# Optimization experiments

Measured on AMD Instinct MI355X. Metric: run time of the kernel, lower is better.

Reference implementation:

```python
import jax, jax.numpy as jnp
import numpy as np

N = 50000        # nodes
E = 800000       # random edges (plus N self-loops added in setup)
DIN = 128        # input_dim
H = 128          # hidden_dim
L = 3            # num_layers
EPS = 1e-5       # BatchNorm1d eps


def _bn(x, gamma, beta):
    # BatchNorm1d in training mode: batch stats over node axis, biased variance
    m = x.mean(axis=0)
    v = jnp.mean((x - m) ** 2, axis=0)
    return (x - m) * jax.lax.rsqrt(v + EPS) * gamma + beta


def setup_inputs() -> dict:
    key = jax.random.key(0)
    ks = jax.random.split(key, 11)
    feats = jax.random.normal(ks[0], (N, DIN), dtype=jnp.float32)
    # edge list with self-loops so every node has degree >= 1 (average pooling divides by degree)
    loops = jnp.arange(N, dtype=jnp.int64)
    src = jnp.concatenate([jax.random.randint(ks[1], (E,), 0, N, dtype=jnp.int64), loops])
    dst = jnp.concatenate([jax.random.randint(ks[2], (E,), 0, N, dtype=jnp.int64), loops])
    s = 0.05
    # per-layer MLP params (num_mlp_layers=2: Linear -> BN -> ReLU -> Linear), layer 0 has DIN==H
    W1 = jax.random.normal(ks[3], (L, DIN, H), dtype=jnp.float32) * s
    b1 = jnp.zeros((L, H), jnp.float32)
    g1 = jnp.ones((L, H), jnp.float32)
    be1 = jnp.zeros((L, H), jnp.float32)
    W2 = jax.random.normal(ks[4], (L, H, H), dtype=jnp.float32) * s
    b2 = jnp.zeros((L, H), jnp.float32)
    # outer BatchNorm1d per GNN layer
    og = jnp.ones((L, H), jnp.float32)
    ob = jnp.zeros((L, H), jnp.float32)
    return {"feats": feats, "W1": W1, "b1": b1, "g1": g1, "be1": be1,
            "W2": W2, "b2": b2, "og": og, "ob": ob, "src": src, "dst": dst}


def reference(feats, W1, b1, g1, be1, W2, b2, og, ob, src, dst):
    n = feats.shape[0]
    # degree = spmm(Adj, ones) -- constant across layers
    deg = jax.ops.segment_sum(jnp.ones(src.shape, jnp.float32), dst, num_segments=n)[:, None]
    h = feats
    for l in range(L):
        # pooled = spmm(Adj, h) via edge gather + segment reduce, then 'average' normalize
        pooled = jax.ops.segment_sum(h[src], dst, num_segments=n) / deg
        # GIN-style 2-layer MLP: Linear -> BN -> ReLU -> Linear
        z = jax.nn.relu(_bn(pooled @ W1[l] + b1[l], g1[l], be1[l]))
        z = z @ W2[l] + b2[l]
        # outer BatchNorm + ReLU
        h = jax.nn.relu(_bn(z, og[l], ob[l]))
    return h
```

## Files before the change

kernel.cpp:

```cpp
#include <hip/hip_runtime.h>
#include <hip/hip_bf16.h>
#include <stdint.h>

typedef _Float16 h16;
typedef h16 h16x2 __attribute__((ext_vector_type(2)));
typedef h16 h16x8 __attribute__((ext_vector_type(8)));
typedef float f32x4 __attribute__((ext_vector_type(4)));

#define HF 128
#define EPS 1e-5f
#define BSH 9
#define BROWS 512
#define BCAP 16384
#define ECHUNK 8192
#define SBANKS 8

union pk32 { uint32_t u; h16x2 h; };

static __device__ __forceinline__ uint32_t pack_h16(float a, float b) {
    pk32 c;
    c.h[0] = (h16)a; c.h[1] = (h16)b;
    return c.u;
}

static __device__ __forceinline__ float sum8(const float* __restrict__ st, int idx) {
    float s = 0.f;
#pragma unroll
    for (int b = 0; b < SBANKS; b++) s += st[b * 256 + idx];
    return s;
}


__global__ __launch_bounds__(256) void k_bscatter(const int* __restrict__ src,
                                                  const int* __restrict__ dst,
                                                  int* __restrict__ gcursor,
                                                  int2* __restrict__ staging, int ne, int nb) {
    __shared__ int h[128], gb[128];
    const int tid = threadIdx.x;
    if (tid < nb) h[tid] = 0;
    __syncthreads();
    const int beg = blockIdx.x * ECHUNK;
    const int end = min(beg + ECHUNK, ne);
    for (int i = beg + tid; i < end; i += 256)
        atomicAdd(&h[dst[i] >> BSH], 1);
    __syncthreads();
    if (tid < nb) {
        int c = h[tid];
        gb[tid] = c ? atomicAdd(&gcursor[tid], c) : 0;
        h[tid] = 0;
    }
    __syncthreads();
    for (int i = beg + tid; i < end; i += 256) {
        int d = dst[i];
        int b = d >> BSH;
        int r = atomicAdd(&h[b], 1);
        staging[(size_t)b * BCAP + gb[b] + r] = make_int2(src[i], d);
    }
}

__global__ __launch_bounds__(256) void k_bbuild(const int2* __restrict__ staging,
                                                const int* __restrict__ gcursor,
                                                int* __restrict__ rowbeg,
                                                int* __restrict__ rowend,
                                                float* __restrict__ deginv,
                                                int* __restrict__ csrsrc, int n) {
    __shared__ int hist[BROWS];
    __shared__ int scan[BROWS];
    const int b = blockIdx.x;
    const int tid = threadIdx.x;
    const int rb = b << BSH;
    const int nrows = min(BROWS, n - rb);
    const int base = b * BCAP;
    const int cnt = gcursor[b];
    hist[tid] = 0; hist[tid + 256] = 0;
    __syncthreads();
    for (int i = tid; i < cnt; i += 256)
        atomicAdd(&hist[staging[base + i].y - rb], 1);
    __syncthreads();
    const int i0 = tid, i1 = tid + 256;
    scan[i0] = hist[i0]; scan[i1] = hist[i1];
    __syncthreads();
    for (int off = 1; off < BROWS; off <<= 1) {
        int v0 = (i0 >= off) ? scan[i0 - off] : 0;
        int v1 = (i1 >= off) ? scan[i1 - off] : 0;
        __syncthreads();
        scan[i0] += v0; scan[i1] += v1;
        __syncthreads();
    }
    for (int r = tid; r < BROWS; r += 256) {
        int c = hist[r];
        int excl = scan[r] - c;
        if (r < nrows) {
            rowbeg[rb + r] = base + excl;
            rowend[rb + r] = base + excl + c;
            deginv[rb + r] = c ? 1.0f / (float)c : 0.f;
        }
        scan[r] = excl;
    }
    __syncthreads();
    for (int i = tid; i < cnt; i += 256) {
        int2 e = staging[base + i];
        int pos = atomicAdd(&scan[e.y - rb], 1);
        csrsrc[base + pos] = e.x;
    }
}

__global__ __launch_bounds__(256) void k_prep(const float* __restrict__ W1,
                                              const float* __restrict__ W2,
                                              h16* __restrict__ wp,
                                              const float* __restrict__ feats,
                                              uint32_t* __restrict__ hbuf, long tot2) {
    const int bid = (int)blockIdx.x;
    if (bid < 384) {
        const int mat = bid >> 6;
        const int idx = ((bid & 63) << 8) + (int)threadIdx.x;
        const int l = mat >> 1;
        const float* Wsrc = (mat & 1) ? (W2 + l * 16384) : (W1 + l * 16384);
        const int nn = idx >> 7, k = idx & 127;
        float w = Wsrc[k * 128 + nn];
        int pos = nn * 128 + ((((k >> 3) ^ (nn & 7))) << 3) + (k & 7);
        wp[mat * 16384 + pos] = (h16)w;
    } else {
        long i = (long)(bid - 384) * 256 + threadIdx.x;
        if (i < tot2) {
            float2 v = ((const float2*)feats)[i];
            hbuf[i] = pack_h16(v.x, v.y);
        }
    }
}

template <int AFF>
__global__ __launch_bounds__(256) void k_spmm(const uint32_t* __restrict__ hp,
                                              const int* __restrict__ rowbeg,
                                              const int* __restrict__ rowend,
                                              const float* __restrict__ deginv,
                                              const float* __restrict__ st,
                                              const float* __restrict__ g,
                                              const float* __restrict__ be,
                                              float inv_n,
                                              const int* __restrict__ csrsrc,
                                              uint32_t* __restrict__ pooled, int n, int np) {
    const int wid  = (int)((blockIdx.x * 256u + threadIdx.x) >> 6);
    const int lane = threadIdx.x & 63;
    if (wid >= np) return;
    uint32_t* outp = pooled + (size_t)wid * 64 + lane;
    if (wid >= n) { *outp = 0u; return; }
    h16x2 s2 = (h16x2)(h16)1.f, c2 = (h16x2)(h16)0.f;
    if (AFF) {
        const int c0 = lane * 2, c1 = c0 + 1;
        float m0 = sum8(st, c0) * inv_n, v0 = sum8(st, 128 + c0) * inv_n - m0 * m0;
        float sx = g[c0] * rsqrtf(v0 + EPS), cx = be[c0] - m0 * sx;
        float m1 = sum8(st, c1) * inv_n, v1 = sum8(st, 128 + c1) * inv_n - m1 * m1;
        float sy = g[c1] * rsqrtf(v1 + EPS), cy = be[c1] - m1 * sy;
        s2[0] = (h16)sx; s2[1] = (h16)sy;
        c2[0] = (h16)cx; c2[1] = (h16)cy;
    }
    const h16 z0 = (h16)0.f;
    h16x2 acc = (h16x2)z0;
    const int beg = rowbeg[wid], end = rowend[wid];
    for (int base = beg; base < end; base += 64) {
        const int rem = end - base;
        const int cnt = rem < 64 ? rem : 64;
        const int off = lane < cnt ? lane : cnt - 1;
        const int idx = csrsrc[base + off];
        int j = 0;
        for (; j + 8 <= cnt; j += 8) {
            uint32_t p[8];
#pragma unroll
            for (int u = 0; u < 8; u++) {
                int s = __builtin_amdgcn_readlane(idx, j + u);
                p[u] = hp[(size_t)s * 64 + lane];
            }
#pragma unroll
            for (int u = 0; u < 8; u++) {
                pk32 w; w.u = p[u];
                h16x2 v = w.h;
                if (AFF) {
                    v = v * s2 + c2;
                    v[0] = v[0] > z0 ? v[0] : z0;
                    v[1] = v[1] > z0 ? v[1] : z0;
                }
                acc = acc + v;
            }
        }
        for (; j < cnt; j++) {
            int s = __builtin_amdgcn_readlane(idx, j);
            pk32 w; w.u = hp[(size_t)s * 64 + lane];
            h16x2 v = w.h;
            if (AFF) {
                v = v * s2 + c2;
                v[0] = v[0] > z0 ? v[0] : z0;
                v[1] = v[1] > z0 ? v[1] : z0;
            }
            acc = acc + v;
        }
    }
    const float di = deginv[wid];
    *outp = pack_h16((float)acc[0] * di, (float)acc[1] * di);
}

template <int MODE>
__global__ __launch_bounds__(256) void k_gemm(const uint32_t* __restrict__ Ap,
                                              const h16* __restrict__ Wp,
                                              const float* __restrict__ bias,
                                              const float* __restrict__ st,
                                              const float* __restrict__ g,
                                              const float* __restrict__ be,
                                              float inv_n,
                                              h16* __restrict__ Y,
                                              float* __restrict__ outstats, int n) {
    __shared__ __align__(16) h16 WT[128 * 128];
    __shared__ float sred[4][128];
    __shared__ float sred2[4][128];
    __shared__ float aff[256];
    const int tid = threadIdx.x;
    const int wave = tid >> 6, lane = tid & 63;

    {
        const char* gsrc = (const char*)Wp + wave * 1024 + lane * 16;
        char* ldst = (char*)&WT[0] + wave * 1024;
#pragma unroll
        for (int i = 0; i < 8; i++) {
            __builtin_amdgcn_global_load_lds(
                (const __attribute__((address_space(1))) uint32_t*)(gsrc + i * 4096),
                (__attribute__((address_space(3))) uint32_t*)(ldst + i * 4096),
                16, 0, 0);
        }
    }
    if (MODE == 1 && tid < 128) {
        float m = sum8(st, tid) * inv_n;
        float v = sum8(st, 128 + tid) * inv_n - m * m;
        float a = g[tid] * rsqrtf(v + EPS);
        aff[tid] = a;
        aff[128 + tid] = be[tid] - m * a;
    }

    const int lrow = lane & 15, quad = lane >> 4;
    const int bx = (int)blockIdx.x * 128;
    int mb[2];
    mb[0] = bx + wave * 16;
    mb[1] = bx + 64 + wave * 16;

    h16x8 ah[2][4];
    uint4 araw[2][4];
#pragma unroll
    for (int rt = 0; rt < 2; rt++) {
        const uint32_t* arow = Ap + (size_t)(mb[rt] + lrow) * 64 + quad * 4;
#pragma unroll
        for (int kt = 0; kt < 4; kt++)
            araw[rt][kt] = *(const uint4*)(arow + kt * 16);
    }

    __syncthreads();

#pragma unroll
    for (int rt = 0; rt < 2; rt++) {
#pragma unroll
        for (int kt = 0; kt < 4; kt++) {
            if (MODE == 0) {
                ah[rt][kt] = *(const h16x8*)&araw[rt][kt];
            } else {
                const uint32_t* pw = (const uint32_t*)&araw[rt][kt];
                h16x8 t;
#pragma unroll
                for (int j2 = 0; j2 < 4; j2++) {
                    pk32 w; w.u = pw[j2];
                    int k = kt * 32 + quad * 8 + j2 * 2;
                    float x0 = fmaxf(fmaf((float)w.h[0], aff[k],     aff[128 + k]),     0.f);
                    float x1 = fmaxf(fmaf((float)w.h[1], aff[k + 1], aff[129 + k]), 0.f);
                    t[2 * j2]     = (h16)x0;
                    t[2 * j2 + 1] = (h16)x1;
                }
                ah[rt][kt] = t;
            }
        }
    }

    f32x4 acc[2][8];
#pragma unroll
    for (int rt = 0; rt < 2; rt++)
#pragma unroll
        for (int nt = 0; nt < 8; nt++) acc[rt][nt] = (f32x4){0.f, 0.f, 0.f, 0.f};

    const int sw = lrow & 7;
#pragma unroll
    for (int nt = 0; nt < 8; nt++) {
        const h16* wbase = &WT[(nt * 16 + lrow) * 128];
#pragma unroll
        for (int kt = 0; kt < 4; kt++) {
            h16x8 bh = *(const h16x8*)(wbase + (((4 * kt + quad) ^ sw) << 3));
#pragma unroll
            for (int rt = 0; rt < 2; rt++)
                acc[rt][nt] = __builtin_amdgcn_mfma_f32_16x16x32_f16(ah[rt][kt], bh, acc[rt][nt], 0, 0, 0);
        }
    }

#pragma unroll
    for (int nt = 0; nt < 8; nt++) {
        int col = nt * 16 + lrow;
        float bv = bias[col];
        float csum = 0.f, csq = 0.f;
#pragma unroll
        for (int rt = 0; rt < 2; rt++) {
#pragma unroll
            for (int r = 0; r < 4; r++) {
                int row = mb[rt] + quad * 4 + r;
                float yv = acc[rt][nt][r] + bv;
                Y[(size_t)row * 128 + col] = (h16)yv;
                if (row < n) { csum += yv; csq += yv * yv; }
            }
        }
        csum += __shfl_xor(csum, 16, 64); csum += __shfl_xor(csum, 32, 64);
        csq  += __shfl_xor(csq,  16, 64); csq  += __shfl_xor(csq,  32, 64);
        if (quad == 0) { sred[wave][col] = csum; sred2[wave][col] = csq; }
    }
    __syncthreads();
    if (tid < 128) {
        float s = sred[0][tid] + sred[1][tid] + sred[2][tid] + sred[3][tid];
        float q = sred2[0][tid] + sred2[1][tid] + sred2[2][tid] + sred2[3][tid];
        const int bank = (int)(blockIdx.x & (SBANKS - 1));
        atomicAdd(&outstats[bank * 256 + tid], s);
        atomicAdd(&outstats[bank * 256 + 128 + tid], q);
    }
}

__global__ __launch_bounds__(256) void k_bnrelu(const uint32_t* __restrict__ Z,
                                                const float* __restrict__ st,
                                                const float* __restrict__ g,
                                                const float* __restrict__ be,
                                                float inv_n,
                                                float* __restrict__ out, long tot2) {
    long i = (long)blockIdx.x * 256 + threadIdx.x;
    if (i >= tot2) return;
    int c = (int)((i * 2) & 127);
    float m0 = sum8(st, c) * inv_n,     v0 = sum8(st, 128 + c) * inv_n - m0 * m0;
    float a0 = g[c] * rsqrtf(v0 + EPS),     c0 = be[c] - m0 * a0;
    float m1 = sum8(st, c + 1) * inv_n, v1 = sum8(st, 129 + c) * inv_n - m1 * m1;
    float a1 = g[c + 1] * rsqrtf(v1 + EPS), c1 = be[c + 1] - m1 * a1;
    pk32 w; w.u = Z[i];
    float2 o;
    o.x = fmaxf(fmaf((float)w.h[0], a0, c0), 0.f);
    o.y = fmaxf(fmaf((float)w.h[1], a1, c1), 0.f);
    ((float2*)out)[i] = o;
}

extern "C" void kernel_launch(void* const* d_in, const int* in_sizes, int n_in,
                              void* d_out, int out_size, void* d_ws, size_t ws_size,
                              hipStream_t stream) {
    const float* feats = (const float*)d_in[0];
    const float* W1    = (const float*)d_in[1];
    const float* b1    = (const float*)d_in[2];
    const float* g1    = (const float*)d_in[3];
    const float* be1   = (const float*)d_in[4];
    const float* W2    = (const float*)d_in[5];
    const float* b2    = (const float*)d_in[6];
    const float* og    = (const float*)d_in[7];
    const float* ob    = (const float*)d_in[8];
    const int*   src   = (const int*)d_in[9];
    const int*   dst   = (const int*)d_in[10];

    const int n  = in_sizes[0] / HF;
    const int ne = in_sizes[9];
    const int np = (n + 127) & ~127;
    const int nb = (n + BROWS - 1) >> BSH;

    char* p = (char*)d_ws;
    auto alloc = [&](size_t bytes) -> char* {
        char* r = p;
        p += (bytes + 511) & ~(size_t)511;
        return r;
    };
    uint32_t* hbuf    = (uint32_t*)alloc((size_t)np * 64 * 4);
    uint32_t* pooled  = (uint32_t*)alloc((size_t)np * 64 * 4);
    uint32_t* ybuf    = (uint32_t*)alloc((size_t)np * 64 * 4);
    uint32_t* zb      = (uint32_t*)alloc((size_t)np * 64 * 4);
    h16*      wprep   = (h16*)     alloc(6 * 16384 * 2);
    float*    deginv  = (float*)   alloc((size_t)n * 4);
    int*      rowbeg  = (int*)     alloc((size_t)n * 4);
    int*      rowend  = (int*)     alloc((size_t)n * 4);
    int*      csrsrc  = (int*)     alloc((size_t)nb * BCAP * 4);
    int2*     staging = (int2*)    alloc((size_t)nb * BCAP * 8);
    char*     zone    = alloc(512 + 6 * SBANKS * 256 * 4);
    int*      gcursor = (int*)zone;
    float*    stats6  = (float*)(zone + 512);

    hipMemsetAsync(zone, 0, 512 + 6 * SBANKS * 256 * 4, stream);

    const long tot2  = (long)n * (HF / 2);
    const int bnb    = (int)((tot2 + 255) / 256);
    const int spmmb  = np / 4;
    const int gemmb  = np / 128;
    const float inv_n = 1.0f / (float)n;
    const int ebk = (ne + ECHUNK - 1) / ECHUNK;
    const int SL = SBANKS * 256;

    k_prep    <<<384 + bnb, 256, 0, stream>>>(W1, W2, wprep, feats, hbuf, tot2);
    k_bscatter<<<ebk, 256, 0, stream>>>(src, dst, gcursor, staging, ne, nb);
    k_bbuild  <<<nb, 256, 0, stream>>>(staging, gcursor, rowbeg, rowend, deginv, csrsrc, n);

    for (int l = 0; l < 3; l++) {
        float* sY = stats6 + (2 * l) * SL;
        float* sZ = stats6 + (2 * l + 1) * SL;
        if (l == 0)
            k_spmm<0><<<spmmb, 256, 0, stream>>>(hbuf, rowbeg, rowend, deginv,
                                                 nullptr, nullptr, nullptr, inv_n,
                                                 csrsrc, pooled, n, np);
        else
            k_spmm<1><<<spmmb, 256, 0, stream>>>(zb, rowbeg, rowend, deginv,
                                                 stats6 + (2 * (l - 1) + 1) * SL,
                                                 og + (l - 1) * HF, ob + (l - 1) * HF, inv_n,
                                                 csrsrc, pooled, n, np);
        k_gemm<0><<<gemmb, 256, 0, stream>>>(pooled,
                                             wprep + (size_t)(2 * l) * 16384,
                                             b1 + l * HF,
                                             nullptr, nullptr, nullptr, inv_n,
                                             (h16*)ybuf, sY, n);
        k_gemm<1><<<gemmb, 256, 0, stream>>>(ybuf,
                                             wprep + (size_t)(2 * l + 1) * 16384,
                                             b2 + l * HF,
                                             sY, g1 + l * HF, be1 + l * HF, inv_n,
                                             (h16*)zb, sZ, n);
    }
    k_bnrelu<<<bnb, 256, 0, stream>>>(zb, stats6 + 5 * SL, og + 2 * HF, ob + 2 * HF,
                                      inv_n, (float*)d_out, tot2);
}
```

Before: 367.7 us.

## Fuse prep into bucket scatter, deepen SpMM unroll, halve GEMM row tile

Merges the weight/feature preparation kernel with the edge bucket-scatter kernel into one launch with block-range dispatch, removing a launch and letting the two independent jobs overlap. Raises the SpMM gather unroll from 8 to 16 rows to keep more loads in flight per wave. Shrinks the GEMM tile from 128 to 64 rows per block, doubling block count and cutting register use, at the cost of loading the weight tile into LDS twice as often.

New measurement: 380.3 us. 1.03x slower.

```diff
diff --git a/kernel.cpp b/kernel.cpp
--- a/kernel.cpp
+++ b/kernel.cpp
@@ -30,31 +30,55 @@
     return s;
 }
 
-
-__global__ __launch_bounds__(256) void k_bscatter(const int* __restrict__ src,
-                                                  const int* __restrict__ dst,
-                                                  int* __restrict__ gcursor,
-                                                  int2* __restrict__ staging, int ne, int nb) {
+__global__ __launch_bounds__(256) void k_front(const int* __restrict__ src,
+                                               const int* __restrict__ dst,
+                                               int* __restrict__ gcursor,
+                                               int2* __restrict__ staging, int ne, int nb,
+                                               const float* __restrict__ W1,
+                                               const float* __restrict__ W2,
+                                               h16* __restrict__ wp,
+                                               const float* __restrict__ feats,
+                                               uint32_t* __restrict__ hbuf, long tot2,
+                                               int ebk) {
     __shared__ int h[128], gb[128];
+    const int bid = (int)blockIdx.x;
     const int tid = threadIdx.x;
-    if (tid < nb) h[tid] = 0;
-    __syncthreads();
-    const int beg = blockIdx.x * ECHUNK;
-    const int end = min(beg + ECHUNK, ne);
-    for (int i = beg + tid; i < end; i += 256)
-        atomicAdd(&h[dst[i] >> BSH], 1);
-    __syncthreads();
-    if (tid < nb) {
-        int c = h[tid];
-        gb[tid] = c ? atomicAdd(&gcursor[tid], c) : 0;
-        h[tid] = 0;
-    }
-    __syncthreads();
-    for (int i = beg + tid; i < end; i += 256) {
-        int d = dst[i];
-        int b = d >> BSH;
-        int r = atomicAdd(&h[b], 1);
-        staging[(size_t)b * BCAP + gb[b] + r] = make_int2(src[i], d);
+    if (bid < ebk) {
+        if (tid < nb) h[tid] = 0;
+        __syncthreads();
+        const int beg = bid * ECHUNK;
+        const int end = min(beg + ECHUNK, ne);
+        for (int i = beg + tid; i < end; i += 256)
+            atomicAdd(&h[dst[i] >> BSH], 1);
+        __syncthreads();
+        if (tid < nb) {
+            int c = h[tid];
+            gb[tid] = c ? atomicAdd(&gcursor[tid], c) : 0;
+            h[tid] = 0;
+        }
+        __syncthreads();
+        for (int i = beg + tid; i < end; i += 256) {
+            int d = dst[i];
+            int b = d >> BSH;
+            int r = atomicAdd(&h[b], 1);
+            staging[(size_t)b * BCAP + gb[b] + r] = make_int2(src[i], d);
+        }
+    } else if (bid < ebk + 384) {
+        const int wb = bid - ebk;
+        const int mat = wb >> 6;
+        const int idx = ((wb & 63) << 8) + tid;
+        const int l = mat >> 1;
+        const float* Wsrc = (mat & 1) ? (W2 + l * 16384) : (W1 + l * 16384);
+        const int nn = idx >> 7, k = idx & 127;
+        float w = Wsrc[k * 128 + nn];
+        int pos = nn * 128 + ((((k >> 3) ^ (nn & 7))) << 3) + (k & 7);
+        wp[mat * 16384 + pos] = (h16)w;
+    } else {
+        long i = (long)(bid - ebk - 384) * 256 + tid;
+        if (i < tot2) {
+            float2 v = ((const float2*)feats)[i];
+            hbuf[i] = pack_h16(v.x, v.y);
+        }
     }
 }
 
@@ -102,30 +126,6 @@
         int2 e = staging[base + i];
         int pos = atomicAdd(&scan[e.y - rb], 1);
         csrsrc[base + pos] = e.x;
-    }
-}
-
-__global__ __launch_bounds__(256) void k_prep(const float* __restrict__ W1,
-                                              const float* __restrict__ W2,
-                                              h16* __restrict__ wp,
-                                              const float* __restrict__ feats,
-                                              uint32_t* __restrict__ hbuf, long tot2) {
-    const int bid = (int)blockIdx.x;
-    if (bid < 384) {
-        const int mat = bid >> 6;
-        const int idx = ((bid & 63) << 8) + (int)threadIdx.x;
-        const int l = mat >> 1;
-        const float* Wsrc = (mat & 1) ? (W2 + l * 16384) : (W1 + l * 16384);
-        const int nn = idx >> 7, k = idx & 127;
-        float w = Wsrc[k * 128 + nn];
-        int pos = nn * 128 + ((((k >> 3) ^ (nn & 7))) << 3) + (k & 7);
-        wp[mat * 16384 + pos] = (h16)w;
-    } else {
-        long i = (long)(bid - 384) * 256 + threadIdx.x;
-        if (i < tot2) {
-            float2 v = ((const float2*)feats)[i];
-            hbuf[i] = pack_h16(v.x, v.y);
-        }
     }
 }
 
@@ -164,15 +164,15 @@
         const int off = lane < cnt ? lane : cnt - 1;
         const int idx = csrsrc[base + off];
         int j = 0;
-        for (; j + 8 <= cnt; j += 8) {
-            uint32_t p[8];
-#pragma unroll
-            for (int u = 0; u < 8; u++) {
+        for (; j + 16 <= cnt; j += 16) {
+            uint32_t p[16];
+#pragma unroll
+            for (int u = 0; u < 16; u++) {
                 int s = __builtin_amdgcn_readlane(idx, j + u);
                 p[u] = hp[(size_t)s * 64 + lane];
             }
 #pragma unroll
-            for (int u = 0; u < 8; u++) {
+            for (int u = 0; u < 16; u++) {
                 pk32 w; w.u = p[u];
                 h16x2 v = w.h;
                 if (AFF) {
@@ -236,51 +236,42 @@
     }
 
     const int lrow = lane & 15, quad = lane >> 4;
-    const int bx = (int)blockIdx.x * 128;
-    int mb[2];
-    mb[0] = bx + wave * 16;
-    mb[1] = bx + 64 + wave * 16;
-
-    h16x8 ah[2][4];
-    uint4 araw[2][4];
-#pragma unroll
-    for (int rt = 0; rt < 2; rt++) {
-        const uint32_t* arow = Ap + (size_t)(mb[rt] + lrow) * 64 + quad * 4;
+    const int mbase = (int)blockIdx.x * 64 + wave * 16;
+
+    uint4 araw[4];
+    {
+        const uint32_t* arow = Ap + (size_t)(mbase + lrow) * 64 + quad * 4;
 #pragma unroll
         for (int kt = 0; kt < 4; kt++)
-            araw[rt][kt] = *(const uint4*)(arow + kt * 16);
-    }
-
-    __syncthreads();
-
-#pragma unroll
-    for (int rt = 0; rt < 2; rt++) {
-#pragma unroll
-        for (int kt = 0; kt < 4; kt++) {
-            if (MODE == 0) {
-                ah[rt][kt] = *(const h16x8*)&araw[rt][kt];
-            } else {
-                const uint32_t* pw = (const uint32_t*)&araw[rt][kt];
-                h16x8 t;
-#pragma unroll
-                for (int j2 = 0; j2 < 4; j2++) {
-                    pk32 w; w.u = pw[j2];
-                    int k = kt * 32 + quad * 8 + j2 * 2;
-                    float x0 = fmaxf(fmaf((float)w.h[0], aff[k],     aff[128 + k]),     0.f);
-                    float x1 = fmaxf(fmaf((float)w.h[1], aff[k + 1], aff[129 + k]), 0.f);
-                    t[2 * j2]     = (h16)x0;
-                    t[2 * j2 + 1] = (h16)x1;
-                }
-                ah[rt][kt] = t;
+            araw[kt] = *(const uint4*)(arow + kt * 16);
+    }
+
+    __syncthreads();
+
+    h16x8 ah[4];
+#pragma unroll
+    for (int kt = 0; kt < 4; kt++) {
+        if (MODE == 0) {
+            ah[kt] = *(const h16x8*)&araw[kt];
+        } else {
+            const uint32_t* pw = (const uint32_t*)&araw[kt];
+            h16x8 t;
+#pragma unroll
+            for (int j2 = 0; j2 < 4; j2++) {
+                pk32 w; w.u = pw[j2];
+                int k = kt * 32 + quad * 8 + j2 * 2;
+                float x0 = fmaxf(fmaf((float)w.h[0], aff[k],     aff[128 + k]), 0.f);
+                float x1 = fmaxf(fmaf((float)w.h[1], aff[k + 1], aff[129 + k]), 0.f);
+                t[2 * j2]     = (h16)x0;
+                t[2 * j2 + 1] = (h16)x1;
             }
-        }
-    }
-
-    f32x4 acc[2][8];
-#pragma unroll
-    for (int rt = 0; rt < 2; rt++)
-#pragma unroll
-        for (int nt = 0; nt < 8; nt++) acc[rt][nt] = (f32x4){0.f, 0.f, 0.f, 0.f};
+            ah[kt] = t;
+        }
+    }
+
+    f32x4 acc[8];
+#pragma unroll
+    for (int nt = 0; nt < 8; nt++) acc[nt] = (f32x4){0.f, 0.f, 0.f, 0.f};
 
     const int sw = lrow & 7;
 #pragma unroll
@@ -289,9 +280,7 @@
 #pragma unroll
         for (int kt = 0; kt < 4; kt++) {
             h16x8 bh = *(const h16x8*)(wbase + (((4 * kt + quad) ^ sw) << 3));
-#pragma unroll
-            for (int rt = 0; rt < 2; rt++)
-                acc[rt][nt] = __builtin_amdgcn_mfma_f32_16x16x32_f16(ah[rt][kt], bh, acc[rt][nt], 0, 0, 0);
+            acc[nt] = __builtin_amdgcn_mfma_f32_16x16x32_f16(ah[kt], bh, acc[nt], 0, 0, 0);
         }
     }
 
@@ -301,14 +290,11 @@
         float bv = bias[col];
         float csum = 0.f, csq = 0.f;
 #pragma unroll
-        for (int rt = 0; rt < 2; rt++) {
-#pragma unroll
-            for (int r = 0; r < 4; r++) {
-                int row = mb[rt] + quad * 4 + r;
-                float yv = acc[rt][nt][r] + bv;
-                Y[(size_t)row * 128 + col] = (h16)yv;
-                if (row < n) { csum += yv; csq += yv * yv; }
-            }
+        for (int r = 0; r < 4; r++) {
+            int row = mbase + quad * 4 + r;
+            float yv = acc[nt][r] + bv;
+            Y[(size_t)row * 128 + col] = (h16)yv;
+            if (row < n) { csum += yv; csq += yv * yv; }
         }
         csum += __shfl_xor(csum, 16, 64); csum += __shfl_xor(csum, 32, 64);
         csq  += __shfl_xor(csq,  16, 64); csq  += __shfl_xor(csq,  32, 64);
@@ -361,7 +347,7 @@
 
     const int n  = in_sizes[0] / HF;
     const int ne = in_sizes[9];
-    const int np = (n + 127) & ~127;
+    const int np = (n + 63) & ~63;
     const int nb = (n + BROWS - 1) >> BSH;
 
     char* p = (char*)d_ws;
@@ -389,14 +375,14 @@
     const long tot2  = (long)n * (HF / 2);
     const int bnb    = (int)((tot2 + 255) / 256);
     const int spmmb  = np / 4;
-    const int gemmb  = np / 128;
+    const int gemmb  = np / 64;
     const float inv_n = 1.0f / (float)n;
     const int ebk = (ne + ECHUNK - 1) / ECHUNK;
     const int SL = SBANKS * 256;
 
-    k_prep    <<<384 + bnb, 256, 0, stream>>>(W1, W2, wprep, feats, hbuf, tot2);
-    k_bscatter<<<ebk, 256, 0, stream>>>(src, dst, gcursor, staging, ne, nb);
-    k_bbuild  <<<nb, 256, 0, stream>>>(staging, gcursor, rowbeg, rowend, deginv, csrsrc, n);
+    k_front <<<ebk + 384 + bnb, 256, 0, stream>>>(src, dst, gcursor, staging, ne, nb,
+                                                  W1, W2, wprep, feats, hbuf, tot2, ebk);
+    k_bbuild<<<nb, 256, 0, stream>>>(staging, gcursor, rowbeg, rowend, deginv, csrsrc, n);
 
     for (int l = 0; l < 3; l++) {
         float* sY = stats6 + (2 * l) * SL;
```
